# Performance work log

Measured on AMD Instinct MI355X. Metric: run time of the kernel, lower is better.

Reference implementation:

```python
import jax, jax.numpy as jnp
import numpy as np
from jax import lax

DN = ('NCDHW', 'OIDHW', 'NCDHW')
ALPHA = 0.1
EPS = 1e-5


def conv3d(x, w, b, padding=1):
    out = lax.conv_general_dilated(x, w, (1, 1, 1), [(padding, padding)] * 3,
                                   dimension_numbers=DN)
    return out + b[None, :, None, None, None]


def conv_transpose3d(x, w, b):
    # PyTorch ConvTranspose3d(k=4, s=2, p=1): equivalent to conv with
    # lhs_dilation=2, flipped kernel, padding k-1-p = 2 per side. Output = 2*D.
    w_c = jnp.flip(jnp.transpose(w, (1, 0, 2, 3, 4)), axis=(2, 3, 4))  # [out,in,4,4,4]
    out = lax.conv_general_dilated(x, w_c, (1, 1, 1), [(2, 2)] * 3,
                                   lhs_dilation=(2, 2, 2), dimension_numbers=DN)
    return out + b[None, :, None, None, None]


def instance_norm(x):
    m = jnp.mean(x, axis=(2, 3, 4), keepdims=True)
    v = jnp.var(x, axis=(2, 3, 4), keepdims=True)
    return (x - m) * lax.rsqrt(v + EPS)


def leaky(x):
    return jnp.where(x >= 0, x, ALPHA * x)


def corr_volume(in1, in2):
    # CorrTorch: 3x3x3 displacement cost volume, mean over channels.
    B, Cc, D, H, W = in1.shape
    in2p = jnp.pad(in2, ((0, 0), (0, 0), (1, 1), (1, 1), (1, 1)))
    vols = []
    for dz in range(3):
        for dy in range(3):
            for dx in range(3):
                win = in2p[:, :, dz:dz + D, dy:dy + H, dx:dx + W]
                vols.append(jnp.mean(in1 * win, axis=1))
    return jnp.stack(vols, axis=1)  # [B, 27, D, H, W]


def setup_inputs() -> dict:
    key = jax.random.key(0)
    ks = jax.random.split(key, 12)
    B, Cf, D = 1, 64, 32  # enc_nf[level-1]=64
    Cin = 3 * 128 + 27    # 411, C channels at level
    Cc = 3 * Cf + 27      # 219
    s = 0.02
    return {
        'src': jax.random.normal(ks[0], (B, Cf, D, D, D), jnp.float32),
        'tgt': jax.random.normal(ks[1], (B, Cf, D, D, D), jnp.float32),
        'C': jax.random.normal(ks[2], (B, Cin, D // 2, D // 2, D // 2), jnp.float32),
        'up_w': jax.random.normal(ks[3], (Cin, Cf, 4, 4, 4), jnp.float32) * s,
        'up_b': jnp.zeros((Cf,), jnp.float32),
        'c1_w': jax.random.normal(ks[4], (Cc, Cc, 3, 3, 3), jnp.float32) * s,
        'c1_b': jnp.zeros((Cc,), jnp.float32),
        'c2_w': jax.random.normal(ks[5], (Cc, Cc, 3, 3, 3), jnp.float32) * s,
        'c2_b': jnp.zeros((Cc,), jnp.float32),
        'out_w': jax.random.normal(ks[6], (3, Cc, 3, 3, 3), jnp.float32) * 1e-5,
        'out_b': jnp.zeros((3,), jnp.float32),
    }


def reference(src, tgt, C, up_w, up_b, c1_w, c1_b, c2_w, c2_b, out_w, out_b):
    Cup = leaky(instance_norm(conv_transpose3d(C, up_w, up_b)))   # upConv
    cost = corr_volume(tgt, src)                                  # CorrTorch(tgt, src)
    x = jnp.concatenate([tgt, src, cost, Cup], axis=1)            # [B,219,D,H,W]
    x = leaky(instance_norm(conv3d(x, c1_w, c1_b)))               # ConvInsBlock 1
    Cn = leaky(instance_norm(conv3d(x, c2_w, c2_b)))              # ConvInsBlock 2
    out = conv3d(Cn, out_w, out_b)                                # flow head
    return (Cn, out)
```

## Files before the change

kernel.cpp:

```cpp
#include <hip/hip_runtime.h>
#include <hip/hip_bf16.h>

#define S3 32768
#define PADD 34
#define PADS (34*34*34)
#define CC 219
#define CF 64
#define CPAD 224
#define CIN_UP 411
#define CUPAD 416
#define ALPHA 0.1f
#define EPS_IN 1e-5f

typedef __attribute__((ext_vector_type(8))) short short8;
typedef __attribute__((ext_vector_type(4))) float floatx4;

__device__ __forceinline__ float lrelu(float v){ return v >= 0.f ? v : ALPHA * v; }
__device__ __forceinline__ unsigned short f2bf(float f){
    unsigned int u = __builtin_bit_cast(unsigned int, f);
    u = (u + 0x7FFFu + ((u >> 16) & 1u)) >> 16;
    return (unsigned short)u;
}
#define LGKM_BARRIER() __asm__ __volatile__("s_waitcnt lgkmcnt(0)\ns_barrier" ::: "memory")

__global__ __launch_bounds__(256) void pad_kernel(const float* __restrict__ src,
                                                  float* __restrict__ dst){
    int idx = blockIdx.x * 256 + threadIdx.x;
    if (idx >= CF * PADS) return;
    int c = idx / PADS, r = idx % PADS;
    int z = r / (PADD*PADD); int r2 = r % (PADD*PADD);
    int y = r2 / PADD, x = r2 % PADD;
    float v = 0.f;
    if (z >= 1 && z <= 32 && y >= 1 && y <= 32 && x >= 1 && x <= 32)
        v = src[((c*32 + (z-1))*32 + (y-1))*32 + (x-1)];
    dst[idx] = v;
}

__global__ __launch_bounds__(256) void corr_kernel(const float* __restrict__ tgt,
                                                   const float* __restrict__ srcp,
                                                   unsigned short* __restrict__ Xp){
    int p = blockIdx.x * 256 + threadIdx.x;
    int z = p >> 10, y = (p >> 5) & 31, x = p & 31;
    float acc[27];
    #pragma unroll
    for (int k = 0; k < 27; k++) acc[k] = 0.f;
    int pbase = ((z+1)*PADD + (y+1))*PADD + (x+1);
    for (int c = 0; c < CF; c++){
        float t = tgt[c*S3 + p];
        const float* sp = srcp + c*PADS + pbase;
        #pragma unroll
        for (int dz = 0; dz < 3; dz++)
            #pragma unroll
            for (int dy = 0; dy < 3; dy++)
                #pragma unroll
                for (int dx = 0; dx < 3; dx++){
                    int k = (dz*3 + dy)*3 + dx;
                    acc[k] += t * sp[(dz-1)*(PADD*PADD) + (dy-1)*PADD + (dx-1)];
                }
    }
    unsigned short cv[27];
    #pragma unroll
    for (int k = 0; k < 27; k++) cv[k] = f2bf(acc[k] * (1.f/64.f));
    size_t bi = ((size_t)(z+1)*1156 + (y+1)*34 + (x+1))*CPAD + 192;
    uint4 o0, o1, o2;
    o0.x = cv[0]  | ((unsigned)cv[1]<<16);  o0.y = cv[2]  | ((unsigned)cv[3]<<16);
    o0.z = cv[4]  | ((unsigned)cv[5]<<16);  o0.w = cv[6]  | ((unsigned)cv[7]<<16);
    o1.x = cv[8]  | ((unsigned)cv[9]<<16);  o1.y = cv[10] | ((unsigned)cv[11]<<16);
    o1.z = cv[12] | ((unsigned)cv[13]<<16); o1.w = cv[14] | ((unsigned)cv[15]<<16);
    o2.x = cv[16] | ((unsigned)cv[17]<<16); o2.y = cv[18] | ((unsigned)cv[19]<<16);
    o2.z = cv[20] | ((unsigned)cv[21]<<16); o2.w = cv[22] | ((unsigned)cv[23]<<16);
    *(uint4*)&Xp[bi]      = o0;
    *(uint4*)&Xp[bi + 8]  = o1;
    *(uint4*)&Xp[bi + 16] = o2;
    *(unsigned int*)&Xp[bi + 24] = cv[24] | ((unsigned)cv[25]<<16);
    Xp[bi + 26] = cv[26];
}

__global__ __launch_bounds__(256) void stats_kernel(const float* __restrict__ xin,
                                                    float* __restrict__ stats, int nch){
    int c = blockIdx.x;
    const float4* p = (const float4*)(xin + (size_t)c * S3);
    float s = 0.f, s2 = 0.f;
    for (int i = threadIdx.x; i < S3/4; i += 256){
        float4 v = p[i];
        s  += v.x + v.y + v.z + v.w;
        s2 += v.x*v.x + v.y*v.y + v.z*v.z + v.w*v.w;
    }
    #pragma unroll
    for (int off = 32; off > 0; off >>= 1){
        s  += __shfl_xor(s,  off);
        s2 += __shfl_xor(s2, off);
    }
    __shared__ float ls[4], ls2[4];
    int wid = threadIdx.x >> 6;
    if ((threadIdx.x & 63) == 0){ ls[wid] = s; ls2[wid] = s2; }
    __syncthreads();
    if (threadIdx.x == 0){
        float S = 0.f, S2 = 0.f;
        #pragma unroll
        for (int w = 0; w < 4; w++){ S += ls[w]; S2 += ls2[w]; }
        float m   = S * (1.f/S3);
        float var = S2 * (1.f/S3) - m*m;
        stats[c]       = m;
        stats[nch + c] = rsqrtf(var + EPS_IN);
    }
}

__global__ __launch_bounds__(256) void norm_apply_kernel(const float* __restrict__ xin,
                                                         const float* __restrict__ stats,
                                                         float* __restrict__ xout, int nch){
    int idx = blockIdx.x * 256 + threadIdx.x;
    int n4  = nch * (S3/4);
    if (idx >= n4) return;
    int c = idx >> 13;
    float m = stats[c], r = stats[nch + c];
    float4 v = ((const float4*)xin)[idx];
    v.x = lrelu((v.x - m) * r);
    v.y = lrelu((v.y - m) * r);
    v.z = lrelu((v.z - m) * r);
    v.w = lrelu((v.w - m) * r);
    ((float4*)xout)[idx] = v;
}

__global__ __launch_bounds__(256) void pack_kernel(const float* __restrict__ src,
        const float* __restrict__ mean, const float* __restrict__ rstd,
        unsigned short* __restrict__ Xp, int Csrc, int dstbase, int donorm){
    __shared__ float sT[64*33];
    const int row = blockIdx.x;
    const int chunk = blockIdx.y;
    const int t = threadIdx.x;
    {
        int c = t >> 2, xq = (t & 3) * 8;
        int csrc = chunk*64 + c;
        float4 v0 = make_float4(0.f,0.f,0.f,0.f), v1 = v0;
        float m = 0.f, r = 1.f;
        if (csrc < Csrc){
            const float4* s4 = (const float4*)&src[(size_t)csrc*S3 + row*32 + xq];
            v0 = s4[0]; v1 = s4[1];
            if (donorm){ m = mean[csrc]; r = rstd[csrc]; }
        }
        if (donorm){
            v0.x = lrelu((v0.x-m)*r); v0.y = lrelu((v0.y-m)*r);
            v0.z = lrelu((v0.z-m)*r); v0.w = lrelu((v0.w-m)*r);
            v1.x = lrelu((v1.x-m)*r); v1.y = lrelu((v1.y-m)*r);
            v1.z = lrelu((v1.z-m)*r); v1.w = lrelu((v1.w-m)*r);
        }
        float* sp = &sT[c*33 + xq];
        sp[0]=v0.x; sp[1]=v0.y; sp[2]=v0.z; sp[3]=v0.w;
        sp[4]=v1.x; sp[5]=v1.y; sp[6]=v1.z; sp[7]=v1.w;
    }
    __syncthreads();
    {
        int x = t >> 3, coff = (t & 7) * 8;
        int dstc = dstbase + chunk*64 + coff;
        if (dstc < CPAD){
            unsigned short u[8];
            #pragma unroll
            for (int j = 0; j < 8; j++) u[j] = f2bf(sT[(coff+j)*33 + x]);
            uint4 o;
            o.x = u[0] | ((unsigned)u[1]<<16);
            o.y = u[2] | ((unsigned)u[3]<<16);
            o.z = u[4] | ((unsigned)u[5]<<16);
            o.w = u[6] | ((unsigned)u[7]<<16);
            int z = row >> 5, y = row & 31;
            size_t pos = (size_t)(z+1)*1156 + (y+1)*34 + (x+1);
            *(uint4*)&Xp[pos*CPAD + dstc] = o;
        }
    }
}

__global__ __launch_bounds__(256) void pack16_kernel(const float* __restrict__ src,
        unsigned short* __restrict__ Cp){
    __shared__ float sT[64*17];
    const int row = blockIdx.x;
    const int chunk = blockIdx.y;
    const int t = threadIdx.x;
    {
        int c = t >> 2, xq = (t & 3) * 4;
        int csrc = chunk*64 + c;
        float4 v = make_float4(0.f,0.f,0.f,0.f);
        if (csrc < CIN_UP)
            v = *(const float4*)&src[(size_t)csrc*4096 + row*16 + xq];
        float* sp = &sT[c*17 + xq];
        sp[0]=v.x; sp[1]=v.y; sp[2]=v.z; sp[3]=v.w;
    }
    __syncthreads();
    {
        int x = t >> 4, coff = (t & 15) * 4;
        int dstc = chunk*64 + coff;
        if (dstc < CUPAD){
            unsigned short u0 = f2bf(sT[(coff+0)*17 + x]);
            unsigned short u1 = f2bf(sT[(coff+1)*17 + x]);
            unsigned short u2 = f2bf(sT[(coff+2)*17 + x]);
            unsigned short u3 = f2bf(sT[(coff+3)*17 + x]);
            uint2 o; o.x = u0 | ((unsigned)u1<<16); o.y = u2 | ((unsigned)u3<<16);
            int z = row >> 4, y = row & 15;
            size_t pos = (size_t)(z+1)*324 + (y+1)*18 + (x+1);
            *(uint2*)&Cp[pos*CUPAD + dstc] = o;
        }
    }
}

__global__ __launch_bounds__(256) void wpack_kernel(const float* __restrict__ w,
        unsigned short* __restrict__ Wt, int perm){
    int idx = blockIdx.x*256 + threadIdx.x;
    int ciin = idx & 31;
    int co   = (idx >> 5) & 255;
    int rest = idx >> 13;
    int cb = rest % 7, tap = rest / 7;
    int ci = cb*32 + ciin;
    float v = 0.f;
    if (co < CC && ci < CC){
        int ciref = ci;
        if (perm) ciref = ci < 128 ? ci : (ci < 192 ? ci + 27 : ci - 64);
        v = w[((size_t)co*CC + ciref)*27 + tap];
    }
    Wt[idx] = f2bf(v);
}

__global__ __launch_bounds__(256) void wpack_out_kernel(const float* __restrict__ w,
        unsigned short* __restrict__ Wt2){
    int idx = blockIdx.x*256 + threadIdx.x;
    if (idx >= 27*7*16*32) return;
    int ciin = idx & 31;
    int co   = (idx >> 5) & 15;
    int rest = idx >> 9;
    int cb = rest % 7, tap = rest / 7;
    int ci = cb*32 + ciin;
    float v = 0.f;
    if (co < 3 && ci < CC)
        v = w[((size_t)co*CC + ci)*27 + tap];
    Wt2[idx] = f2bf(v);
}

__global__ __launch_bounds__(256) void wupack_kernel(const float* __restrict__ w,
        unsigned short* __restrict__ Wu){
    int idx = blockIdx.x*256 + threadIdx.x;
    int ci = idx % CUPAD;
    int rest = idx / CUPAD;
    int co = rest & 63;
    int pj = rest >> 6;
    int j = pj & 7, p = pj >> 3;
    float v = 0.f;
    if (ci < CIN_UP){
        int oz = p>>2, oy = (p>>1)&1, ox = p&1;
        int jz = j>>2, jy = (j>>1)&1, jx = j&1;
        int wz = 3 - oz - 2*jz, wy = 3 - oy - 2*jy, wx = 3 - ox - 2*jx;
        v = w[(((size_t)ci*64 + co)*64) + wz*16 + wy*4 + wx];
    }
    Wu[idx] = f2bf(v);
}

__global__ __launch_bounds__(256,2) void ups_mfma_kernel(const unsigned short* __restrict__ Cp,
        const unsigned short* __restrict__ Wu, float* __restrict__ U){
    __shared__ unsigned short sA[64*40];
    __shared__ unsigned short sB[64*40];
    const int nt = blockIdx.x;
    const int p  = nt >> 6;
    const int zp = (nt >> 2) & 15;
    const int y0 = (nt & 3) * 4;
    const int oz = p>>2, oy = (p>>1)&1, ox = p&1;
    const int t = threadIdx.x, w = t>>6, l = t&63;
    const int mw = (w&1)*32, nw = (w>>1)*32;
    const int lm = l&15, lq = l>>4;
    const int sn = t>>2, spart = (t&3)*8;
    const int sr = sn>>4, sx = sn&15;
    floatx4 acc[2][2];
    #pragma unroll
    for (int i=0;i<2;i++)
        #pragma unroll
        for (int j=0;j<2;j++) acc[i][j] = (floatx4){0.f,0.f,0.f,0.f};

    for (int j = 0; j < 8; ++j){
        int sz = oz + (j>>2), sy = oy + ((j>>1)&1), sxx = ox + (j&1);
        size_t pbase = ((size_t)(zp+sz)*324 + (y0+sr+sy)*18 + (sx+sxx)) * CUPAD;
        size_t abase = ((size_t)(p*8 + j)*64 + sn)*CUPAD;
        for (int cb = 0; cb < 13; ++cb){
            uint4 av = *(const uint4*)&Wu[abase + cb*32 + spart];
            uint4 bv = *(const uint4*)&Cp[pbase + cb*32 + spart];
            *(uint4*)&sA[sn*40 + spart] = av;
            *(uint4*)&sB[sn*40 + spart] = bv;
            __syncthreads();
            short8 af[2], bfv[2];
            #pragma unroll
            for (int i=0;i<2;i++){
                af[i]  = *(const short8*)&sA[(mw + i*16 + lm)*40 + lq*8];
                bfv[i] = *(const short8*)&sB[(nw + i*16 + lm)*40 + lq*8];
            }
            #pragma unroll
            for (int i=0;i<2;i++)
                #pragma unroll
                for (int jj=0;jj<2;jj++)
                    acc[i][jj] = __builtin_amdgcn_mfma_f32_16x16x32_bf16(af[i], bfv[jj], acc[i][jj], 0,0,0);
            __syncthreads();
        }
    }
    #pragma unroll
    for (int i=0;i<2;i++){
        #pragma unroll
        for (int jj=0;jj<2;jj++){
            int n = nw + jj*16 + lm;
            int yy = y0 + (n>>4), xx = n&15;
            size_t opos = ((size_t)(2*zp+oz)<<10) + ((size_t)(2*yy+oy)<<5) + (2*xx+ox);
            #pragma unroll
            for (int r=0;r<4;r++){
                int co = mw + i*16 + lq*4 + r;
                U[(size_t)co*S3 + opos] = acc[i][jj][r];
            }
        }
    }
}

__global__ __launch_bounds__(256,2) void conv_mfma_kernel(const unsigned short* __restrict__ Xp,
        const unsigned short* __restrict__ Wt, const float* __restrict__ bg,
        float* __restrict__ Y){
    __shared__ unsigned short sB[612*40];
    const int nt = blockIdx.x;
    const int mt = blockIdx.y;
    const int z  = nt >> 3;
    const int y0 = (nt & 7) * 4;
    const int t = threadIdx.x, w = t>>6, l = t&63;
    const int mw = (w & 1) * 64, nw = (w >> 1) * 64;
    const int lm = l & 15, lq = l >> 4;
    const unsigned short* ap = Wt + (size_t)(mt*128 + mw + lm)*32 + lq*8;

    int vB[4];
    #pragma unroll
    for (int j=0;j<4;j++){
        int n = nw + j*16 + lm;
        vB[j] = ((n>>5)*34 + (n&31))*80 + lq*16;
    }
    unsigned int goff[10]; int loff[10];
    #pragma unroll
    for (int k=0;k<10;k++){
        int idx = t + k*256;
        int p = idx >> 2, q = idx & 3;
        int zz = p / 204, rem = p % 204;
        int yy = rem / 34, x = rem - yy*34;
        goff[k] = (unsigned)((((z+zz)*1156 + (y0+yy)*34 + x)*CPAD + q*8) * 2);
        loff[k] = (p*40 + q*8) * 2;
    }
    const bool full9 = (t < 144);

    floatx4 acc[4][4];
    #pragma unroll
    for (int i=0;i<4;i++)
        #pragma unroll
        for (int j=0;j<4;j++) acc[i][j] = (floatx4){0.f,0.f,0.f,0.f};

    short8 Aq[2][4];
    short8 bf[2][4];

    for (int cb = 0; cb < 7; ++cb){
        const unsigned short* apc = ap + (size_t)cb*8192;
        #pragma unroll
        for (int i=0;i<4;i++) Aq[0][i] = *(const short8*)(apc + i*512);
        #pragma unroll
        for (int i=0;i<4;i++) Aq[1][i] = *(const short8*)(apc + (size_t)57344 + i*512);

        const char* gb = (const char*)Xp + cb*64;
        LGKM_BARRIER();
        #pragma unroll
        for (int k=0;k<9;k++){
            uint4 v = *(const uint4*)(gb + goff[k]);
            *(uint4*)((char*)sB + loff[k]) = v;
        }
        if (full9){
            uint4 v = *(const uint4*)(gb + goff[9]);
            *(uint4*)((char*)sB + loff[9]) = v;
        }
        LGKM_BARRIER();

        #pragma unroll
        for (int j=0;j<4;j++) bf[0][j] = *(const short8*)((const char*)sB + vB[j]);

        #define TAP_BODY(TAP, PAR) do{                                                   \
            const int tap_ = (TAP);                                                      \
            if (tap_ < 26){                                                              \
                int t1 = tap_ + 1;                                                       \
                int toff1 = ((t1/9)*204 + ((t1/3)%3)*34 + (t1%3))*80;                    \
                _Pragma("unroll")                                                        \
                for (int j=0;j<4;j++)                                                    \
                    bf[(PAR)^1][j] = *(const short8*)((const char*)sB + (vB[j] + toff1));\
            }                                                                            \
            _Pragma("unroll")                                                            \
            for (int i=0;i<4;i++)                                                        \
                _Pragma("unroll")                                                        \
                for (int j=0;j<4;j++)                                                    \
                    acc[i][j] = __builtin_amdgcn_mfma_f32_16x16x32_bf16(                 \
                        Aq[PAR][i], bf[PAR][j], acc[i][j], 0,0,0);                       \
            if (tap_ < 25){                                                              \
                const unsigned short* pn = apc + (size_t)(tap_+2)*57344;                 \
                _Pragma("unroll")                                                        \
                for (int i=0;i<4;i++) Aq[PAR][i] = *(const short8*)(pn + i*512);         \
            }                                                                            \
        }while(0)

        #pragma unroll 1
        for (int pr = 0; pr < 13; ++pr){
            int tap = pr*2;
            TAP_BODY(tap,   0);
            TAP_BODY(tap+1, 1);
        }
        TAP_BODY(26, 0);
        #undef TAP_BODY
    }
    #pragma unroll
    for (int i=0;i<4;i++){
        #pragma unroll
        for (int j=0;j<4;j++){
            const int n = nw + j*16 + lm;
            const size_t pp = ((size_t)z<<10) + ((size_t)(y0 + (n>>5))<<5) + (n&31);
            #pragma unroll
            for (int r=0;r<4;r++){
                int gm = mt*128 + mw + i*16 + lq*4 + r;
                if (gm < CC) Y[(size_t)gm*S3 + pp] = acc[i][j][r] + bg[gm];
            }
        }
    }
}

__global__ __launch_bounds__(256,2) void convout_mfma_kernel(const unsigned short* __restrict__ Xp,
        const unsigned short* __restrict__ Wt2, const float* __restrict__ bgl,
        float* __restrict__ Y){
    __shared__ unsigned short sB[612*36];
    const int nt = blockIdx.x;
    const int z  = nt >> 3;
    const int y0 = (nt & 7) * 4;
    const int t = threadIdx.x, w = t>>6, l = t&63;
    const int nw = w * 32;
    const int lm = l & 15, lq = l >> 4;
    floatx4 acc[2];
    acc[0] = (floatx4){0.f,0.f,0.f,0.f};
    acc[1] = (floatx4){0.f,0.f,0.f,0.f};

    for (int cb = 0; cb < 7; ++cb){
        __syncthreads();
        for (int idx = t; idx < 2448; idx += 256){
            int p = idx >> 2, q = idx & 3;
            int zz = p / 204, rem = p % 204;
            int yy = rem / 34, x = rem - yy*34;
            uint4 v = *(const uint4*)&Xp[((size_t)((z+zz)*1156 + (y0+yy)*34 + x))*CPAD + cb*32 + q*8];
            *(uint4*)&sB[p*36 + q*8] = v;
        }
        short8 af[27];
        {
            const unsigned short* wp = Wt2 + ((size_t)(cb*16 + lm))*32 + lq*8;
            #pragma unroll
            for (int tap = 0; tap < 27; ++tap)
                af[tap] = *(const short8*)(wp + (size_t)tap*3584);
        }
        __syncthreads();
        #pragma unroll
        for (int tap = 0; tap < 27; ++tap){
            const int dz = tap/9, dy = (tap/3)%3, dx = tap%3;
            #pragma unroll
            for (int j=0;j<2;j++){
                int n = nw + j*16 + lm;
                int r = n >> 5, x = n & 31;
                short8 bf = *(const short8*)&sB[(dz*204 + (r+dy)*34 + (x+dx))*36 + lq*8];
                acc[j] = __builtin_amdgcn_mfma_f32_16x16x32_bf16(af[tap], bf, acc[j], 0,0,0);
            }
        }
    }
    if (lq == 0){
        #pragma unroll
        for (int j = 0; j < 2; j++){
            int n = nw + j*16 + lm;
            size_t pp = ((size_t)z<<10) + ((size_t)(y0 + (n>>5))<<5) + (n&31);
            #pragma unroll
            for (int r = 0; r < 3; r++)
                Y[(size_t)r*S3 + pp] = acc[j][r] + bgl[r];
        }
    }
}

extern "C" void kernel_launch(void* const* d_in, const int* in_sizes, int n_in,
                              void* d_out, int out_size, void* d_ws, size_t ws_size,
                              hipStream_t stream) {
    const float* src   = (const float*)d_in[0];
    const float* tgt   = (const float*)d_in[1];
    const float* Cmat  = (const float*)d_in[2];
    const float* up_w  = (const float*)d_in[3];
    const float* c1_w  = (const float*)d_in[5];
    const float* c1_b  = (const float*)d_in[6];
    const float* c2_w  = (const float*)d_in[7];
    const float* c2_b  = (const float*)d_in[8];
    const float* out_w = (const float*)d_in[9];
    const float* out_b = (const float*)d_in[10];

    float* out = (float*)d_out;
    char* ws = (char*)d_ws;
    unsigned short* Xp = (unsigned short*)ws;
    float*  U  = (float*)(ws + 17608192);
    unsigned short* Wt = (unsigned short*)(ws + 17608192);
    unsigned short* Cp = (unsigned short*)(ws + 25996800);
    unsigned short* Wu = (unsigned short*)(ws + 25996800 + 4852224);
    float* srcp = (float*)(ws + 25996800);
    unsigned short* Wt2 = (unsigned short*)(ws + 25996800);
    float* stats = (float*)(ws + 36058624);

    hipMemsetAsync(Xp, 0, 17608192, stream);
    hipMemsetAsync(Cp, 0, 4852224, stream);

    pack16_kernel<<<dim3(256,7), 256, 0, stream>>>(Cmat, Cp);
    wupack_kernel<<<6656, 256, 0, stream>>>(up_w, Wu);
    ups_mfma_kernel<<<512, 256, 0, stream>>>(Cp, Wu, U);
    stats_kernel<<<64, 256, 0, stream>>>(U, stats, 64);
    pack_kernel<<<dim3(1024,1), 256, 0, stream>>>(U, stats, stats+64, Xp, 64, 128, 1);
    pack_kernel<<<dim3(1024,1), 256, 0, stream>>>(tgt, nullptr, nullptr, Xp, 64, 0, 0);
    pack_kernel<<<dim3(1024,1), 256, 0, stream>>>(src, nullptr, nullptr, Xp, 64, 64, 0);
    pad_kernel<<<9826, 256, 0, stream>>>(src, srcp);
    corr_kernel<<<128, 256, 0, stream>>>(tgt, srcp, Xp);
    wpack_out_kernel<<<378, 256, 0, stream>>>(out_w, Wt2);
    wpack_kernel<<<6048, 256, 0, stream>>>(c1_w, Wt, 1);
    conv_mfma_kernel<<<dim3(256,2), 256, 0, stream>>>(Xp, Wt, c1_b, out);
    stats_kernel<<<219, 256, 0, stream>>>(out, stats, 219);
    pack_kernel<<<dim3(1024,4), 256, 0, stream>>>(out, stats, stats+219, Xp, 219, 0, 1);
    wpack_kernel<<<6048, 256, 0, stream>>>(c2_w, Wt, 0);
    conv_mfma_kernel<<<dim3(256,2), 256, 0, stream>>>(Xp, Wt, c2_b, out);
    stats_kernel<<<219, 256, 0, stream>>>(out, stats, 219);
    pack_kernel<<<dim3(1024,4), 256, 0, stream>>>(out, stats, stats+219, Xp, 219, 0, 1);
    norm_apply_kernel<<<(219*(S3/4))/256, 256, 0, stream>>>(out, stats, out, 219);
    convout_mfma_kernel<<<256, 256, 0, stream>>>(Xp, Wt2, out_b, out + (size_t)CC*S3);
}
```

Baseline: 552.7 us.

## Deepen conv MFMA prefetch to three stages, fuse norm-apply into pack, resize corr blocks

The main conv kernel now keeps three register buffers for the A weights and B LDS fragments, prefetching two taps ahead instead of one. It also raises wave priority around the MFMA block with s_setprio. The final pack kernel now writes the normalized fp32 output in place, which removes the separate norm_apply pass over the 219-channel tensor. The correlation kernel moves to 128-thread blocks with twice as many blocks, for better CU coverage. The deeper prefetch adds VGPR pressure that could reduce occupancy or cause spills under launch_bounds(256,2).

```diff
diff --git a/kernel.cpp b/kernel.cpp
--- a/kernel.cpp
+++ b/kernel.cpp
@@ -36,10 +36,10 @@
     dst[idx] = v;
 }
 
-__global__ __launch_bounds__(256) void corr_kernel(const float* __restrict__ tgt,
+__global__ __launch_bounds__(128) void corr_kernel(const float* __restrict__ tgt,
                                                    const float* __restrict__ srcp,
                                                    unsigned short* __restrict__ Xp){
-    int p = blockIdx.x * 256 + threadIdx.x;
+    int p = blockIdx.x * 128 + threadIdx.x;
     int z = p >> 10, y = (p >> 5) & 31, x = p & 31;
     float acc[27];
     #pragma unroll
@@ -106,25 +106,10 @@
     }
 }
 
-__global__ __launch_bounds__(256) void norm_apply_kernel(const float* __restrict__ xin,
-                                                         const float* __restrict__ stats,
-                                                         float* __restrict__ xout, int nch){
-    int idx = blockIdx.x * 256 + threadIdx.x;
-    int n4  = nch * (S3/4);
-    if (idx >= n4) return;
-    int c = idx >> 13;
-    float m = stats[c], r = stats[nch + c];
-    float4 v = ((const float4*)xin)[idx];
-    v.x = lrelu((v.x - m) * r);
-    v.y = lrelu((v.y - m) * r);
-    v.z = lrelu((v.z - m) * r);
-    v.w = lrelu((v.w - m) * r);
-    ((float4*)xout)[idx] = v;
-}
-
 __global__ __launch_bounds__(256) void pack_kernel(const float* __restrict__ src,
         const float* __restrict__ mean, const float* __restrict__ rstd,
-        unsigned short* __restrict__ Xp, int Csrc, int dstbase, int donorm){
+        unsigned short* __restrict__ Xp, float* __restrict__ fp32out,
+        int Csrc, int dstbase, int donorm){
     __shared__ float sT[64*33];
     const int row = blockIdx.x;
     const int chunk = blockIdx.y;
@@ -144,6 +129,10 @@
             v0.z = lrelu((v0.z-m)*r); v0.w = lrelu((v0.w-m)*r);
             v1.x = lrelu((v1.x-m)*r); v1.y = lrelu((v1.y-m)*r);
             v1.z = lrelu((v1.z-m)*r); v1.w = lrelu((v1.w-m)*r);
+        }
+        if (fp32out && csrc < Csrc){
+            float4* o4 = (float4*)&fp32out[(size_t)csrc*S3 + row*32 + xq];
+            o4[0] = v0; o4[1] = v1;
         }
         float* sp = &sT[c*33 + xq];
         sp[0]=v0.x; sp[1]=v0.y; sp[2]=v0.z; sp[3]=v0.w;
@@ -348,8 +337,8 @@
         #pragma unroll
         for (int j=0;j<4;j++) acc[i][j] = (floatx4){0.f,0.f,0.f,0.f};
 
-    short8 Aq[2][4];
-    short8 bf[2][4];
+    short8 Aq[3][4];
+    short8 bf[3][4];
 
     for (int cb = 0; cb < 7; ++cb){
         const unsigned short* apc = ap + (size_t)cb*8192;
@@ -357,6 +346,8 @@
         for (int i=0;i<4;i++) Aq[0][i] = *(const short8*)(apc + i*512);
         #pragma unroll
         for (int i=0;i<4;i++) Aq[1][i] = *(const short8*)(apc + (size_t)57344 + i*512);
+        #pragma unroll
+        for (int i=0;i<4;i++) Aq[2][i] = *(const short8*)(apc + (size_t)2*57344 + i*512);
 
         const char* gb = (const char*)Xp + cb*64;
         LGKM_BARRIER();
@@ -373,36 +364,40 @@
 
         #pragma unroll
         for (int j=0;j<4;j++) bf[0][j] = *(const short8*)((const char*)sB + vB[j]);
+        #pragma unroll
+        for (int j=0;j<4;j++) bf[1][j] = *(const short8*)((const char*)sB + (vB[j] + 80));
 
         #define TAP_BODY(TAP, PAR) do{                                                   \
             const int tap_ = (TAP);                                                      \
-            if (tap_ < 26){                                                              \
-                int t1 = tap_ + 1;                                                       \
-                int toff1 = ((t1/9)*204 + ((t1/3)%3)*34 + (t1%3))*80;                    \
+            if (tap_ < 25){                                                              \
+                int t2 = tap_ + 2;                                                       \
+                int toff2 = ((t2/9)*204 + ((t2/3)%3)*34 + (t2%3))*80;                    \
                 _Pragma("unroll")                                                        \
                 for (int j=0;j<4;j++)                                                    \
-                    bf[(PAR)^1][j] = *(const short8*)((const char*)sB + (vB[j] + toff1));\
+                    bf[((PAR)+2)%3][j] = *(const short8*)((const char*)sB + (vB[j] + toff2));\
             }                                                                            \
+            __builtin_amdgcn_s_setprio(1);                                               \
             _Pragma("unroll")                                                            \
             for (int i=0;i<4;i++)                                                        \
                 _Pragma("unroll")                                                        \
                 for (int j=0;j<4;j++)                                                    \
                     acc[i][j] = __builtin_amdgcn_mfma_f32_16x16x32_bf16(                 \
                         Aq[PAR][i], bf[PAR][j], acc[i][j], 0,0,0);                       \
-            if (tap_ < 25){                                                              \
-                const unsigned short* pn = apc + (size_t)(tap_+2)*57344;                 \
+            __builtin_amdgcn_s_setprio(0);                                               \
+            if (tap_ < 24){                                                              \
+                const unsigned short* pn = apc + (size_t)(tap_+3)*57344;                 \
                 _Pragma("unroll")                                                        \
                 for (int i=0;i<4;i++) Aq[PAR][i] = *(const short8*)(pn + i*512);         \
             }                                                                            \
         }while(0)
 
         #pragma unroll 1
-        for (int pr = 0; pr < 13; ++pr){
-            int tap = pr*2;
+        for (int pr = 0; pr < 9; ++pr){
+            int tap = pr*3;
             TAP_BODY(tap,   0);
             TAP_BODY(tap+1, 1);
-        }
-        TAP_BODY(26, 0);
+            TAP_BODY(tap+2, 2);
+        }
         #undef TAP_BODY
     }
     #pragma unroll
@@ -507,20 +502,19 @@
     wupack_kernel<<<6656, 256, 0, stream>>>(up_w, Wu);
     ups_mfma_kernel<<<512, 256, 0, stream>>>(Cp, Wu, U);
     stats_kernel<<<64, 256, 0, stream>>>(U, stats, 64);
-    pack_kernel<<<dim3(1024,1), 256, 0, stream>>>(U, stats, stats+64, Xp, 64, 128, 1);
-    pack_kernel<<<dim3(1024,1), 256, 0, stream>>>(tgt, nullptr, nullptr, Xp, 64, 0, 0);
-    pack_kernel<<<dim3(1024,1), 256, 0, stream>>>(src, nullptr, nullptr, Xp, 64, 64, 0);
+    pack_kernel<<<dim3(1024,1), 256, 0, stream>>>(U, stats, stats+64, Xp, nullptr, 64, 128, 1);
+    pack_kernel<<<dim3(1024,1), 256, 0, stream>>>(tgt, nullptr, nullptr, Xp, nullptr, 64, 0, 0);
+    pack_kernel<<<dim3(1024,1), 256, 0, stream>>>(src, nullptr, nullptr, Xp, nullptr, 64, 64, 0);
     pad_kernel<<<9826, 256, 0, stream>>>(src, srcp);
-    corr_kernel<<<128, 256, 0, stream>>>(tgt, srcp, Xp);
+    corr_kernel<<<256, 128, 0, stream>>>(tgt, srcp, Xp);
     wpack_out_kernel<<<378, 256, 0, stream>>>(out_w, Wt2);
     wpack_kernel<<<6048, 256, 0, stream>>>(c1_w, Wt, 1);
     conv_mfma_kernel<<<dim3(256,2), 256, 0, stream>>>(Xp, Wt, c1_b, out);
     stats_kernel<<<219, 256, 0, stream>>>(out, stats, 219);
-    pack_kernel<<<dim3(1024,4), 256, 0, stream>>>(out, stats, stats+219, Xp, 219, 0, 1);
+    pack_kernel<<<dim3(1024,4), 256, 0, stream>>>(out, stats, stats+219, Xp, nullptr, 219, 0, 1);
     wpack_kernel<<<6048, 256, 0, stream>>>(c2_w, Wt, 0);
     conv_mfma_kernel<<<dim3(256,2), 256, 0, stream>>>(Xp, Wt, c2_b, out);
     stats_kernel<<<219, 256, 0, stream>>>(out, stats, 219);
-    pack_kernel<<<dim3(1024,4), 256, 0, stream>>>(out, stats, stats+219, Xp, 219, 0, 1);
-    norm_apply_kernel<<<(219*(S3/4))/256, 256, 0, stream>>>(out, stats, out, 219);
+    pack_kernel<<<dim3(1024,4), 256, 0, stream>>>(out, stats, stats+219, Xp, out, 219, 0, 1);
     convout_mfma_kernel<<<256, 256, 0, stream>>>(Xp, Wt2, out_b, out + (size_t)CC*S3);
 }
```

Measured after the change: 541.3 us. 1.02x faster.
